# Kernel tuning notes

Measured on AMD Instinct MI355X. Metric: run time of the kernel, lower is better.

The kernel has to match this reference:

```python
import jax, jax.numpy as jnp
import numpy as np

B, N, IN_DIM, HEADS, PER_HEAD = 8, 512, 256, 4, 32
OUT_DIM = HEADS * PER_HEAD  # 128
NEG_SLOPE = 0.2


def setup_inputs() -> dict:
    key = jax.random.key(0)
    ks = jax.random.split(key, 8)
    x = jax.random.normal(ks[0], (B, N, IN_DIM), jnp.float32)
    adj = jax.random.randint(ks[1], (B, N, N), 0, 2, jnp.int32)
    sl = 1.0 / np.sqrt(IN_DIM)
    W_l = jax.random.normal(ks[2], (IN_DIM, OUT_DIM), jnp.float32) * sl  # source proj
    b_l = jnp.zeros((OUT_DIM,), jnp.float32)
    W_r = jax.random.normal(ks[3], (IN_DIM, OUT_DIM), jnp.float32) * sl  # target proj
    b_r = jnp.zeros((OUT_DIM,), jnp.float32)
    att = jax.random.normal(ks[4], (HEADS, PER_HEAD), jnp.float32) * (1.0 / np.sqrt(PER_HEAD))
    bias = jnp.zeros((OUT_DIM,), jnp.float32)
    return {"x": x, "adj": adj, "W_l": W_l, "b_l": b_l, "W_r": W_r, "b_r": b_r,
            "att": att, "bias": bias}


def _gatv2_single(x_b, adj_b, W_l, b_l, W_r, b_r, att, bias):
    # PyG GATv2Conv: remove_self_loops + add_self_loops -> diagonal forced to 1
    n = x_b.shape[0]
    adj_sl = jnp.fill_diagonal(adj_b, 1, inplace=False)
    # edge_index = adj.nonzero().t(): source = row, target = col
    m = (adj_sl != 0).T  # m[i, j]: source j feeds target i
    xl = (x_b @ W_l + b_l).reshape(n, HEADS, PER_HEAD)  # source-side features
    xr = (x_b @ W_r + b_r).reshape(n, HEADS, PER_HEAD)  # target-side features
    s = xr[:, None] + xl[None, :]                       # [i, j, H, C]
    s = jnp.where(s > 0, s, NEG_SLOPE * s)              # LeakyReLU(0.2)
    e = jnp.einsum('ijhc,hc->ijh', s, att)              # attention logits
    e = jnp.where(m[..., None], e, -jnp.inf)
    alpha = jax.nn.softmax(e, axis=1)                   # softmax over sources j
    out = jnp.einsum('ijh,jhc->ihc', alpha, xl).reshape(n, HEADS * PER_HEAD)
    return out + bias


def reference(x, adj, W_l, b_l, W_r, b_r, att, bias):
    # Sequential per-batch processing, faithful to the original Python loop
    # and keeping the [N,N,H,C] intermediate to one graph at a time.
    def one(args):
        x_b, adj_b = args
        return _gatv2_single(x_b, adj_b, W_l, b_l, W_r, b_r, att, bias)
    return jax.lax.map(one, (x, adj))  # [B, N, OUT_DIM]
```

## Files before the change

kernel.cpp:

```cpp
#include <hip/hip_runtime.h>

#define B_   8
#define N_   512
#define IND  256
#define H_   4
#define PH   32
#define OD   128
#define TI   4

typedef float v2f __attribute__((ext_vector_type(2)));

#define ATT_SCALE 0.5770780163555854f
#define DLR_SCALE 0.8656170245333781f

template <int PAT>
__device__ __forceinline__ float dpp_add(float x) {
    int yi = __builtin_amdgcn_mov_dpp(__float_as_int(x), PAT, 0xF, 0xF, true);
    return x + __int_as_float(yi);
}

__device__ __forceinline__ float fast_exp2(float x) {
#if __has_builtin(__builtin_amdgcn_exp2f)
    return __builtin_amdgcn_exp2f(x);
#else
    return exp2f(x);
#endif
}

__device__ __forceinline__ void pk_fma(v2f& d, v2f a, v2f b) {
    asm("v_pk_fma_f32 %0, %1, %2, %0" : "+v"(d) : "v"(a), "v"(b));
}

__global__ __launch_bounds__(512, 2) void proj_kernel(
    const float* __restrict__ x,
    const float* __restrict__ Wl, const float* __restrict__ bl,
    const float* __restrict__ Wr, const float* __restrict__ br,
    const float* __restrict__ att,
    float* __restrict__ xl, float* __restrict__ xr,
    float* __restrict__ dl, float* __restrict__ dr)
{
    __shared__ float xs[8 * IND];
    __shared__ float comb[8][64][33];

    const int t = threadIdx.x;
    const int row0 = blockIdx.x * 8;

    ((float4*)xs)[t] = ((const float4*)(x + (size_t)row0 * IND))[t];
    __syncthreads();

    const int og    = t & 31;
    const int ks    = (t >> 5) & 7;
    const int which = t >> 8;
    const int o0 = og * 4;
    const int k0 = ks * 32;
    const float* W = (which ? Wr : Wl) + (size_t)k0 * OD + o0;

    float acc[8][4];
    #pragma unroll
    for (int r = 0; r < 8; ++r)
        #pragma unroll
        for (int c = 0; c < 4; ++c) acc[r][c] = 0.f;

    float4 wb[2][4];
    #pragma unroll
    for (int kk = 0; kk < 4; ++kk)
        wb[0][kk] = *(const float4*)(W + (size_t)kk * OD);

    #pragma unroll 2
    for (int s = 0; s < 8; ++s) {
        const int cur = s & 1, nxt = cur ^ 1;
        if (s < 7) {
            const float* Wq = W + (size_t)((s + 1) * 4) * OD;
            #pragma unroll
            for (int kk = 0; kk < 4; ++kk)
                wb[nxt][kk] = *(const float4*)(Wq + (size_t)kk * OD);
        }
        float4 xv[8];
        #pragma unroll
        for (int r = 0; r < 8; ++r)
            xv[r] = *(const float4*)(&xs[r * IND + k0 + s * 4]);
        #pragma unroll
        for (int kk = 0; kk < 4; ++kk) {
            #pragma unroll
            for (int r = 0; r < 8; ++r) {
                const float xk = (kk == 0) ? xv[r].x : (kk == 1) ? xv[r].y
                               : (kk == 2) ? xv[r].z : xv[r].w;
                acc[r][0] = fmaf(xk, wb[cur][kk].x, acc[r][0]);
                acc[r][1] = fmaf(xk, wb[cur][kk].y, acc[r][1]);
                acc[r][2] = fmaf(xk, wb[cur][kk].z, acc[r][2]);
                acc[r][3] = fmaf(xk, wb[cur][kk].w, acc[r][3]);
            }
        }
    }

    const int pid = og | (which << 5);
    #pragma unroll
    for (int i = 0; i < 32; ++i)
        comb[ks][pid][i] = acc[i >> 2][i & 3];
    __syncthreads();

    const int ogf = t & 31;
    const int rf  = (t >> 5) & 7;
    const int whf = t >> 8;
    const int pidf = ogf | (whf << 5);
    const float* bb = whf ? br : bl;
    float* dst = whf ? xr : xl;
    float* dp  = whf ? dr : dl;
    float4 bv = *(const float4*)(bb + ogf * 4);
    float4 av = *(const float4*)(att + ogf * 4);
    const float bvf[4] = {bv.x, bv.y, bv.z, bv.w};
    const float avf[4] = {av.x, av.y, av.z, av.w};
    float y[4];
    #pragma unroll
    for (int c = 0; c < 4; ++c) {
        const int idx = rf * 4 + c;
        float s01 = comb[0][pidf][idx] + comb[1][pidf][idx];
        float s23 = comb[2][pidf][idx] + comb[3][pidf][idx];
        float s45 = comb[4][pidf][idx] + comb[5][pidf][idx];
        float s67 = comb[6][pidf][idx] + comb[7][pidf][idx];
        y[c] = ((s01 + s23) + (s45 + s67)) + bvf[c];
    }
    *(float4*)(&dst[(size_t)(row0 + rf) * OD + ogf * 4]) =
        make_float4(y[0], y[1], y[2], y[3]);
    float dc = fmaf(avf[0], y[0], fmaf(avf[1], y[1],
               fmaf(avf[2], y[2], avf[3] * y[3])));
    dc += __shfl_xor(dc, 1);
    dc += __shfl_xor(dc, 2);
    dc += __shfl_xor(dc, 4);
    if ((ogf & 7) == 0)
        dp[(size_t)(row0 + rf) * H_ + (ogf >> 3)] = DLR_SCALE * dc;
}

__global__ __launch_bounds__(256, 4) void attn_kernel(
    const int* __restrict__ adj, const float* __restrict__ att,
    const float* __restrict__ bias,
    const float* __restrict__ xl, const float* __restrict__ xr,
    const float* __restrict__ dl, const float* __restrict__ dr,
    float* __restrict__ out)
{
    const int t = threadIdx.x;
    const int bid = (blockIdx.x & 7) * 128 + (blockIdx.x >> 3);
    const int b  = bid >> 7;
    const int i0 = (bid & 127) * TI;
    const int cq = t & 3;
    const int h  = t >> 6;
    const int js = (t >> 2) & 15;
    const int cbase = h * PH + cq * 8;

    float atS[8];
    {
        const float* ap = att + cbase;
        float4 a0 = *(const float4*)(ap);
        float4 a1 = *(const float4*)(ap + 4);
        atS[0] = ATT_SCALE * a0.x; atS[1] = ATT_SCALE * a0.y;
        atS[2] = ATT_SCALE * a0.z; atS[3] = ATT_SCALE * a0.w;
        atS[4] = ATT_SCALE * a1.x; atS[5] = ATT_SCALE * a1.y;
        atS[6] = ATT_SCALE * a1.z; atS[7] = ATT_SCALE * a1.w;
    }
    float xrS[TI][8];
    float drv[TI];
    #pragma unroll
    for (int il = 0; il < TI; ++il) {
        const float* xp = xr + ((size_t)(b * N_ + i0 + il)) * OD + cbase;
        float4 r0 = *(const float4*)(xp);
        float4 r1 = *(const float4*)(xp + 4);
        xrS[il][0] = r0.x; xrS[il][1] = r0.y; xrS[il][2] = r0.z; xrS[il][3] = r0.w;
        xrS[il][4] = r1.x; xrS[il][5] = r1.y; xrS[il][6] = r1.z; xrS[il][7] = r1.w;
        drv[il] = dr[((size_t)(b * N_ + i0 + il)) * H_ + h];
    }

    v2f acc[TI][4];
    float sumw[TI];
    #pragma unroll
    for (int il = 0; il < TI; ++il) {
        sumw[il] = 0.f;
        #pragma unroll
        for (int m = 0; m < 4; ++m) acc[il][m] = (v2f){0.f, 0.f};
    }

    const float* xlp = xl + ((size_t)(b * N_ + js)) * OD + cbase;
    const int*   ajp = adj + ((size_t)(b * N_ + js)) * N_ + i0;
    const float* dlp = dl + ((size_t)(b * N_ + js)) * H_ + h;

    #pragma unroll 2
    for (int u = 0; u < 32; ++u) {
        float4 wa = *(const float4*)(xlp);
        float4 wb = *(const float4*)(xlp + 4);
        int4   wm = *(const int4*)(ajp);
        float  wd = *dlp;
        xlp += 16 * OD; ajp += 16 * N_; dlp += 16 * H_;

        const int j = u * 16 + js;
        v2f p0 = (v2f){wa.x, wa.y}, p1 = (v2f){wa.z, wa.w};
        v2f p2 = (v2f){wb.x, wb.y}, p3 = (v2f){wb.z, wb.w};
        int wmv[TI] = {wm.x, wm.y, wm.z, wm.w};
        #pragma unroll
        for (int il = 0; il < TI; ++il) {
            float s, e2a = 0.f, e2b = 0.f;
            s = xrS[il][0] + wa.x; e2a = fmaf(atS[0], __builtin_fabsf(s), e2a);
            s = xrS[il][1] + wa.y; e2b = fmaf(atS[1], __builtin_fabsf(s), e2b);
            s = xrS[il][2] + wa.z; e2a = fmaf(atS[2], __builtin_fabsf(s), e2a);
            s = xrS[il][3] + wa.w; e2b = fmaf(atS[3], __builtin_fabsf(s), e2b);
            s = xrS[il][4] + wb.x; e2a = fmaf(atS[4], __builtin_fabsf(s), e2a);
            s = xrS[il][5] + wb.y; e2b = fmaf(atS[5], __builtin_fabsf(s), e2b);
            s = xrS[il][6] + wb.z; e2a = fmaf(atS[6], __builtin_fabsf(s), e2a);
            s = xrS[il][7] + wb.w; e2b = fmaf(atS[7], __builtin_fabsf(s), e2b);
            float eh = e2a + e2b;
            eh = dpp_add<0xB1>(eh);
            eh = dpp_add<0x4E>(eh);
            float e = (wd + drv[il]) + eh;
            bool keep = (wmv[il] != 0) || (j == i0 + il);
            float w = keep ? fast_exp2(e) : 0.f;
            sumw[il] += w;
            v2f ws = (v2f){w, w};
            pk_fma(acc[il][0], ws, p0);
            pk_fma(acc[il][1], ws, p1);
            pk_fma(acc[il][2], ws, p2);
            pk_fma(acc[il][3], ws, p3);
        }
    }

    #pragma unroll
    for (int m = 4; m <= 32; m <<= 1) {
        #pragma unroll
        for (int il = 0; il < TI; ++il) {
            sumw[il] += __shfl_xor(sumw[il], m);
            #pragma unroll
            for (int q = 0; q < 4; ++q) {
                acc[il][q].x += __shfl_xor(acc[il][q].x, m);
                acc[il][q].y += __shfl_xor(acc[il][q].y, m);
            }
        }
    }

    const int g = js;
    if (g < 8) {
        const int il  = g >> 1;
        const int hf  = g & 1;
        const float inv = 1.f / sumw[il];
        const int c0 = cbase + hf * 4;
        float4 bq = *(const float4*)(bias + c0);
        v2f a0 = acc[il][2 * hf], a1 = acc[il][2 * hf + 1];
        float4 vout = make_float4(fmaf(a0.x, inv, bq.x),
                                  fmaf(a0.y, inv, bq.y),
                                  fmaf(a1.x, inv, bq.z),
                                  fmaf(a1.y, inv, bq.w));
        *(float4*)(&out[((size_t)(b * N_ + i0 + il)) * OD + c0]) = vout;
    }
}

extern "C" void kernel_launch(void* const* d_in, const int* in_sizes, int n_in,
                              void* d_out, int out_size, void* d_ws, size_t ws_size,
                              hipStream_t stream) {
    const float* x    = (const float*)d_in[0];
    const int*   adj  = (const int*)d_in[1];
    const float* Wl   = (const float*)d_in[2];
    const float* bl   = (const float*)d_in[3];
    const float* Wr   = (const float*)d_in[4];
    const float* br   = (const float*)d_in[5];
    const float* att  = (const float*)d_in[6];
    const float* bias = (const float*)d_in[7];
    float* out = (float*)d_out;

    float* xl = (float*)d_ws;
    float* xr = xl + (size_t)B_ * N_ * OD;
    float* dl = xr + (size_t)B_ * N_ * OD;
    float* dr = dl + (size_t)B_ * N_ * H_;

    proj_kernel<<<512, 512, 0, stream>>>(x, Wl, bl, Wr, br, att, xl, xr, dl, dr);
    attn_kernel<<<1024, 256, 0, stream>>>(adj, att, bias, xl, xr, dl, dr, out);
}
```

Measured before the change: 127.8 us.

## Re-split GATv2 kernels: wider attention blocks, LDS reduction, prefetch, drop target term

The projection kernel now uses 4-row, 256-thread blocks, twice as many blocks, and a longer k-slice per thread. The attention kernel grows to 512 threads with 32 source slices per head, so each thread runs half as many loop iterations. Next-iteration operands are prefetched into registers, and the long shuffle-reduction chain is replaced by an LDS reduction in two passes. The per-target logit term dr is dropped because softmax over sources does not change when a per-target constant is added. In exchange the kernel uses more LDS and extra barriers, and the float4 LDS stores go to a 33-float padded row stride, so some of them are not 16-byte aligned.

```diff
diff --git a/kernel.cpp b/kernel.cpp
--- a/kernel.cpp
+++ b/kernel.cpp
@@ -31,7 +31,7 @@
     asm("v_pk_fma_f32 %0, %1, %2, %0" : "+v"(d) : "v"(a), "v"(b));
 }
 
-__global__ __launch_bounds__(512, 2) void proj_kernel(
+__global__ __launch_bounds__(256, 4) void proj_kernel(
     const float* __restrict__ x,
     const float* __restrict__ Wl, const float* __restrict__ bl,
     const float* __restrict__ Wr, const float* __restrict__ br,
@@ -39,69 +39,63 @@
     float* __restrict__ xl, float* __restrict__ xr,
     float* __restrict__ dl, float* __restrict__ dr)
 {
-    __shared__ float xs[8 * IND];
-    __shared__ float comb[8][64][33];
+    __shared__ float xs[4 * IND];
+    __shared__ float comb[4][64][17];
 
     const int t = threadIdx.x;
-    const int row0 = blockIdx.x * 8;
+    const int row0 = blockIdx.x * 4;
 
     ((float4*)xs)[t] = ((const float4*)(x + (size_t)row0 * IND))[t];
     __syncthreads();
 
     const int og    = t & 31;
-    const int ks    = (t >> 5) & 7;
-    const int which = t >> 8;
+    const int ks    = (t >> 5) & 3;
+    const int which = t >> 7;
     const int o0 = og * 4;
-    const int k0 = ks * 32;
+    const int k0 = ks * 64;
     const float* W = (which ? Wr : Wl) + (size_t)k0 * OD + o0;
 
-    float acc[8][4];
-    #pragma unroll
-    for (int r = 0; r < 8; ++r)
+    float acc[4][4];
+    #pragma unroll
+    for (int r = 0; r < 4; ++r)
         #pragma unroll
         for (int c = 0; c < 4; ++c) acc[r][c] = 0.f;
 
-    float4 wb[2][4];
-    #pragma unroll
-    for (int kk = 0; kk < 4; ++kk)
-        wb[0][kk] = *(const float4*)(W + (size_t)kk * OD);
+    float4 wb[2][2];
+    wb[0][0] = *(const float4*)(W);
+    wb[0][1] = *(const float4*)(W + OD);
 
     #pragma unroll 2
-    for (int s = 0; s < 8; ++s) {
+    for (int s = 0; s < 32; ++s) {
         const int cur = s & 1, nxt = cur ^ 1;
-        if (s < 7) {
-            const float* Wq = W + (size_t)((s + 1) * 4) * OD;
-            #pragma unroll
-            for (int kk = 0; kk < 4; ++kk)
-                wb[nxt][kk] = *(const float4*)(Wq + (size_t)kk * OD);
-        }
-        float4 xv[8];
-        #pragma unroll
-        for (int r = 0; r < 8; ++r)
-            xv[r] = *(const float4*)(&xs[r * IND + k0 + s * 4]);
-        #pragma unroll
-        for (int kk = 0; kk < 4; ++kk) {
-            #pragma unroll
-            for (int r = 0; r < 8; ++r) {
-                const float xk = (kk == 0) ? xv[r].x : (kk == 1) ? xv[r].y
-                               : (kk == 2) ? xv[r].z : xv[r].w;
-                acc[r][0] = fmaf(xk, wb[cur][kk].x, acc[r][0]);
-                acc[r][1] = fmaf(xk, wb[cur][kk].y, acc[r][1]);
-                acc[r][2] = fmaf(xk, wb[cur][kk].z, acc[r][2]);
-                acc[r][3] = fmaf(xk, wb[cur][kk].w, acc[r][3]);
-            }
+        if (s < 31) {
+            const float* Wq = W + (size_t)(2 * (s + 1)) * OD;
+            wb[nxt][0] = *(const float4*)(Wq);
+            wb[nxt][1] = *(const float4*)(Wq + OD);
+        }
+        #pragma unroll
+        for (int r = 0; r < 4; ++r) {
+            float2 xv = *(const float2*)(&xs[r * IND + k0 + 2 * s]);
+            acc[r][0] = fmaf(xv.x, wb[cur][0].x, acc[r][0]);
+            acc[r][1] = fmaf(xv.x, wb[cur][0].y, acc[r][1]);
+            acc[r][2] = fmaf(xv.x, wb[cur][0].z, acc[r][2]);
+            acc[r][3] = fmaf(xv.x, wb[cur][0].w, acc[r][3]);
+            acc[r][0] = fmaf(xv.y, wb[cur][1].x, acc[r][0]);
+            acc[r][1] = fmaf(xv.y, wb[cur][1].y, acc[r][1]);
+            acc[r][2] = fmaf(xv.y, wb[cur][1].z, acc[r][2]);
+            acc[r][3] = fmaf(xv.y, wb[cur][1].w, acc[r][3]);
         }
     }
 
     const int pid = og | (which << 5);
     #pragma unroll
-    for (int i = 0; i < 32; ++i)
+    for (int i = 0; i < 16; ++i)
         comb[ks][pid][i] = acc[i >> 2][i & 3];
     __syncthreads();
 
     const int ogf = t & 31;
-    const int rf  = (t >> 5) & 7;
-    const int whf = t >> 8;
+    const int rf  = (t >> 5) & 3;
+    const int whf = t >> 7;
     const int pidf = ogf | (whf << 5);
     const float* bb = whf ? br : bl;
     float* dst = whf ? xr : xl;
@@ -114,11 +108,8 @@
     #pragma unroll
     for (int c = 0; c < 4; ++c) {
         const int idx = rf * 4 + c;
-        float s01 = comb[0][pidf][idx] + comb[1][pidf][idx];
-        float s23 = comb[2][pidf][idx] + comb[3][pidf][idx];
-        float s45 = comb[4][pidf][idx] + comb[5][pidf][idx];
-        float s67 = comb[6][pidf][idx] + comb[7][pidf][idx];
-        y[c] = ((s01 + s23) + (s45 + s67)) + bvf[c];
+        y[c] = ((comb[0][pidf][idx] + comb[1][pidf][idx])
+              + (comb[2][pidf][idx] + comb[3][pidf][idx])) + bvf[c];
     }
     *(float4*)(&dst[(size_t)(row0 + rf) * OD + ogf * 4]) =
         make_float4(y[0], y[1], y[2], y[3]);
@@ -131,20 +122,23 @@
         dp[(size_t)(row0 + rf) * H_ + (ogf >> 3)] = DLR_SCALE * dc;
 }
 
-__global__ __launch_bounds__(256, 4) void attn_kernel(
+__global__ __launch_bounds__(512, 4) void attn_kernel(
     const int* __restrict__ adj, const float* __restrict__ att,
     const float* __restrict__ bias,
     const float* __restrict__ xl, const float* __restrict__ xr,
     const float* __restrict__ dl, const float* __restrict__ dr,
     float* __restrict__ out)
 {
+    __shared__ float sacc[H_][2][32][PH + 1];
+    __shared__ float ssum[H_][32][TI];
+
     const int t = threadIdx.x;
     const int bid = (blockIdx.x & 7) * 128 + (blockIdx.x >> 3);
     const int b  = bid >> 7;
     const int i0 = (bid & 127) * TI;
     const int cq = t & 3;
-    const int h  = t >> 6;
-    const int js = (t >> 2) & 15;
+    const int js = (t >> 2) & 31;
+    const int h  = t >> 7;
     const int cbase = h * PH + cq * 8;
 
     float atS[8];
@@ -158,7 +152,6 @@
         atS[6] = ATT_SCALE * a1.z; atS[7] = ATT_SCALE * a1.w;
     }
     float xrS[TI][8];
-    float drv[TI];
     #pragma unroll
     for (int il = 0; il < TI; ++il) {
         const float* xp = xr + ((size_t)(b * N_ + i0 + il)) * OD + cbase;
@@ -166,7 +159,6 @@
         float4 r1 = *(const float4*)(xp + 4);
         xrS[il][0] = r0.x; xrS[il][1] = r0.y; xrS[il][2] = r0.z; xrS[il][3] = r0.w;
         xrS[il][4] = r1.x; xrS[il][5] = r1.y; xrS[il][6] = r1.z; xrS[il][7] = r1.w;
-        drv[il] = dr[((size_t)(b * N_ + i0 + il)) * H_ + h];
     }
 
     v2f acc[TI][4];
@@ -182,15 +174,24 @@
     const int*   ajp = adj + ((size_t)(b * N_ + js)) * N_ + i0;
     const float* dlp = dl + ((size_t)(b * N_ + js)) * H_ + h;
 
+    float4 va = *(const float4*)(xlp);
+    float4 vb = *(const float4*)(xlp + 4);
+    int4   mj = *(const int4*)(ajp);
+    float  dj = *dlp;
+
     #pragma unroll 2
-    for (int u = 0; u < 32; ++u) {
-        float4 wa = *(const float4*)(xlp);
-        float4 wb = *(const float4*)(xlp + 4);
-        int4   wm = *(const int4*)(ajp);
-        float  wd = *dlp;
-        xlp += 16 * OD; ajp += 16 * N_; dlp += 16 * H_;
-
-        const int j = u * 16 + js;
+    for (int u = 0; u < 16; ++u) {
+        float4 wa = va, wb = vb;
+        int4   wm = mj;
+        float  wd = dj;
+        if (u < 15) {
+            xlp += 32 * OD; ajp += 32 * N_; dlp += 32 * H_;
+            va = *(const float4*)(xlp);
+            vb = *(const float4*)(xlp + 4);
+            mj = *(const int4*)(ajp);
+            dj = *dlp;
+        }
+        const int j = u * 32 + js;
         v2f p0 = (v2f){wa.x, wa.y}, p1 = (v2f){wa.z, wa.w};
         v2f p2 = (v2f){wb.x, wb.y}, p3 = (v2f){wb.z, wb.w};
         int wmv[TI] = {wm.x, wm.y, wm.z, wm.w};
@@ -208,7 +209,7 @@
             float eh = e2a + e2b;
             eh = dpp_add<0xB1>(eh);
             eh = dpp_add<0x4E>(eh);
-            float e = (wd + drv[il]) + eh;
+            float e = wd + eh;
             bool keep = (wmv[il] != 0) || (j == i0 + il);
             float w = keep ? fast_exp2(e) : 0.f;
             sumw[il] += w;
@@ -220,32 +221,57 @@
         }
     }
 
-    #pragma unroll
-    for (int m = 4; m <= 32; m <<= 1) {
-        #pragma unroll
-        for (int il = 0; il < TI; ++il) {
-            sumw[il] += __shfl_xor(sumw[il], m);
-            #pragma unroll
-            for (int q = 0; q < 4; ++q) {
-                acc[il][q].x += __shfl_xor(acc[il][q].x, m);
-                acc[il][q].y += __shfl_xor(acc[il][q].y, m);
-            }
-        }
-    }
-
-    const int g = js;
-    if (g < 8) {
-        const int il  = g >> 1;
-        const int hf  = g & 1;
-        const float inv = 1.f / sumw[il];
-        const int c0 = cbase + hf * 4;
-        float4 bq = *(const float4*)(bias + c0);
-        v2f a0 = acc[il][2 * hf], a1 = acc[il][2 * hf + 1];
-        float4 vout = make_float4(fmaf(a0.x, inv, bq.x),
-                                  fmaf(a0.y, inv, bq.y),
-                                  fmaf(a1.x, inv, bq.z),
-                                  fmaf(a1.y, inv, bq.w));
-        *(float4*)(&out[((size_t)(b * N_ + i0 + il)) * OD + c0]) = vout;
+    if (cq == 0) {
+        #pragma unroll
+        for (int il = 0; il < TI; ++il)
+            ssum[h][js][il] = sumw[il];
+    }
+    #pragma unroll
+    for (int p = 0; p < 2; ++p) {
+        *(float4*)(&sacc[h][p][js][cq * 8]) =
+            make_float4(acc[p][0].x, acc[p][0].y, acc[p][1].x, acc[p][1].y);
+        *(float4*)(&sacc[h][p][js][cq * 8 + 4]) =
+            make_float4(acc[p][2].x, acc[p][2].y, acc[p][3].x, acc[p][3].y);
+    }
+    __syncthreads();
+    if (t < 256) {
+        const int c   = t & 31;
+        const int ilr = (t >> 5) & 1;
+        const int hr  = t >> 6;
+        float a = 0.f, st = 0.f;
+        #pragma unroll
+        for (int k = 0; k < 32; ++k) {
+            a  += sacc[hr][ilr][k][c];
+            st += ssum[hr][k][ilr];
+        }
+        const int cg = hr * PH + c;
+        out[((size_t)(b * N_ + i0 + ilr)) * OD + cg] =
+            fmaf(a, 1.f / st, bias[cg]);
+    }
+    __syncthreads();
+    #pragma unroll
+    for (int p = 0; p < 2; ++p) {
+        *(float4*)(&sacc[h][p][js][cq * 8]) =
+            make_float4(acc[2 + p][0].x, acc[2 + p][0].y,
+                        acc[2 + p][1].x, acc[2 + p][1].y);
+        *(float4*)(&sacc[h][p][js][cq * 8 + 4]) =
+            make_float4(acc[2 + p][2].x, acc[2 + p][2].y,
+                        acc[2 + p][3].x, acc[2 + p][3].y);
+    }
+    __syncthreads();
+    if (t < 256) {
+        const int c   = t & 31;
+        const int ilr = (t >> 5) & 1;
+        const int hr  = t >> 6;
+        float a = 0.f, st = 0.f;
+        #pragma unroll
+        for (int k = 0; k < 32; ++k) {
+            a  += sacc[hr][ilr][k][c];
+            st += ssum[hr][k][2 + ilr];
+        }
+        const int cg = hr * PH + c;
+        out[((size_t)(b * N_ + i0 + 2 + ilr)) * OD + cg] =
+            fmaf(a, 1.f / st, bias[cg]);
     }
 }
 
@@ -267,6 +293,6 @@
     float* dl = xr + (size_t)B_ * N_ * OD;
     float* dr = dl + (size_t)B_ * N_ * H_;
 
-    proj_kernel<<<512, 512, 0, stream>>>(x, Wl, bl, Wr, br, att, xl, xr, dl, dr);
-    attn_kernel<<<1024, 256, 0, stream>>>(adj, att, bias, xl, xr, dl, dr, out);
-}
+    proj_kernel<<<1024, 256, 0, stream>>>(x, Wl, bl, Wr, br, att, xl, xr, dl, dr);
+    attn_kernel<<<1024, 512, 0, stream>>>(adj, att, bias, xl, xr, dl, dr, out);
+}
```

New measurement: 121.0 us. 5.3% less time.
